# Performance work log

Hardware: AMD Instinct MI355X
Metric: run time of the kernel (lower is better)

## Reference

```python
import jax, jax.numpy as jnp
import numpy as np


def setup_inputs() -> dict:
    key = jax.random.key(0)
    k0, k1, k2, k3, k4 = jax.random.split(key, 5)
    T, B, I, H = 1024, 128, 256, 256
    x = jax.random.normal(k0, (T, B, I), dtype=jnp.float32)
    h0 = jax.random.normal(k1, (1, B, H), dtype=jnp.float32)
    # prepacked transposed weights, gate order [r|z|n] along the 3H axis
    wihT = jax.random.normal(k2, (I, 3 * H), dtype=jnp.float32) * 0.05
    whhT = jax.random.normal(k3, (H, 3 * H), dtype=jnp.float32) * 0.05
    b = jax.random.normal(k4, (3 * H,), dtype=jnp.float32) * 0.05  # fused b_ih + b_hh
    return {"x": x, "h0": h0, "wihT": wihT, "whhT": whhT, "b": b}


def reference(x, h0, wihT, whhT, b):
    # Single-layer GRU recurrence, matching the fused CUDA kernel math:
    #   r = sigmoid(x Wir + h Whr + b_r)
    #   z = sigmoid(x Wiz + h Whz + b_z)
    #   h' = (1 - z) * n + z * h
    H = h0.shape[-1]
    br, bz, bn = b[:H], b[H:2 * H], b[2 * H:]

    def step(h, xt):
        gi = xt @ wihT   # (B, 3H)
        gh = h @ whhT    # (B, 3H)
        r = jax.nn.sigmoid(gi[:, :H] + gh[:, :H] + br)
        z = jax.nn.sigmoid(gi[:, H:2 * H] + gh[:, H:2 * H] + bz)
        n = jnp.tanh(gi[:, 2 * H:] + bn + r * gh[:, 2 * H:])
        h_new = (1.0 - z) * n + z * h
        return h_new, None

    h_final, _ = jax.lax.scan(step, h0[0], x)  # scan over T
    return h_final[None]  # (1, B, H)
```

## Files before the change

### kernel.cpp

```cpp
#include <hip/hip_runtime.h>
#include <hip/hip_fp16.h>

#define TT 1024
#define BB 128
#define II 256
#define HH 256
#define NG 768

__device__ __align__(16) unsigned short g_xbf[(size_t)TT * BB * II];
__device__ __align__(16) unsigned short g_wihB[NG * II];
__device__ __align__(16) _Float16       g_gi[(size_t)TT * BB * NG];

typedef __attribute__((ext_vector_type(8))) short    bfrag;
typedef __attribute__((ext_vector_type(8))) _Float16 hfrag;
typedef __attribute__((ext_vector_type(4))) float    f32x4;

__device__ __forceinline__ unsigned short f2bf(float f) {
    unsigned u = __float_as_uint(f);
    return (unsigned short)((u + 0x7fffu + ((u >> 16) & 1u)) >> 16);
}

__global__ void cvt_x_kernel(const float* __restrict__ x) {
    const int n4 = TT * BB * II / 4;
    for (int i = blockIdx.x * blockDim.x + threadIdx.x; i < n4;
         i += gridDim.x * blockDim.x) {
        float4 v = reinterpret_cast<const float4*>(x)[i];
        ushort4 o;
        o.x = f2bf(v.x); o.y = f2bf(v.y); o.z = f2bf(v.z); o.w = f2bf(v.w);
        reinterpret_cast<ushort4*>(g_xbf)[i] = o;
    }
}

__global__ void cvt_wih_kernel(const float* __restrict__ wihT) {
    const int n = blockIdx.x;
    const int k = threadIdx.x;
    g_wihB[n * II + k] = f2bf(wihT[k * NG + n]);
}

__global__ void __launch_bounds__(256) gi_gemm_kernel(const float* __restrict__ bias) {
    __shared__ unsigned short Ab[128 * 32];
    __shared__ unsigned short Bb[128 * 32];
    const int tid = threadIdx.x;
    const int mt = blockIdx.x / 6, nt = blockIdx.x % 6;
    const int m0 = mt * 128, n0 = nt * 128;
    const int l = tid & 63, w = tid >> 6;
    const int wr = w >> 1, wc = w & 1;
    const int srow = tid >> 2, scol = (tid & 3) * 8;

    f32x4 acc[4][4] = {};

    for (int ks = 0; ks < 8; ++ks) {
        const int k0 = ks * 32;
        __syncthreads();
        #pragma unroll
        for (int c = 0; c < 2; ++c) {
            const int row = c * 64 + srow;
            *reinterpret_cast<uint4*>(&Ab[row * 32 + scol]) =
                *reinterpret_cast<const uint4*>(&g_xbf[(size_t)(m0 + row) * II + k0 + scol]);
            *reinterpret_cast<uint4*>(&Bb[row * 32 + scol]) =
                *reinterpret_cast<const uint4*>(&g_wihB[(n0 + row) * II + k0 + scol]);
        }
        __syncthreads();
        bfrag af[4], bf[4];
        #pragma unroll
        for (int i = 0; i < 4; ++i) {
            af[i] = *reinterpret_cast<const bfrag*>(
                        &Ab[(wr * 64 + i * 16 + (l & 15)) * 32 + (l >> 4) * 8]);
            bf[i] = *reinterpret_cast<const bfrag*>(
                        &Bb[(wc * 64 + i * 16 + (l & 15)) * 32 + (l >> 4) * 8]);
        }
        #pragma unroll
        for (int mi = 0; mi < 4; ++mi)
            #pragma unroll
            for (int ni = 0; ni < 4; ++ni)
                acc[mi][ni] = __builtin_amdgcn_mfma_f32_16x16x32_bf16(
                                  af[mi], bf[ni], acc[mi][ni], 0, 0, 0);
    }
    #pragma unroll
    for (int mi = 0; mi < 4; ++mi) {
        const int grow = m0 + wr * 64 + mi * 16 + (l >> 4) * 4;
        #pragma unroll
        for (int ni = 0; ni < 4; ++ni) {
            const int gcol = n0 + wc * 64 + ni * 16 + (l & 15);
            const float bv = bias[gcol];
            #pragma unroll
            for (int q = 0; q < 4; ++q)
                g_gi[(size_t)(grow + q) * NG + gcol] = (_Float16)(acc[mi][ni][q] + bv);
        }
    }
}

#define LDB(NAME, CB, KT)                                                   \
    hfrag NAME;                                                             \
    _Pragma("unroll")                                                       \
    for (int e = 0; e < 8; ++e)                                             \
        NAME[e] = (_Float16)whhT[(size_t)((KT) * 32 + g * 8 + e) * NG + (CB) + ln15];

#define KSTEP(KT)                                                           \
    {                                                                       \
        const hfrag Av = *reinterpret_cast<const hfrag*>(hl + (KT) * 32 + (g << 3)); \
        const hfrag A  = (ln15 == 0) ? Av : hz;                             \
        accR = __builtin_amdgcn_mfma_f32_16x16x32_f16(A, BR##KT, accR, 0, 0, 0); \
        accZ = __builtin_amdgcn_mfma_f32_16x16x32_f16(A, BZ##KT, accZ, 0, 0, 0); \
        accN = __builtin_amdgcn_mfma_f32_16x16x32_f16(A, BN##KT, accN, 0, 0, 0); \
    }

__global__ void __launch_bounds__(1024)
__attribute__((amdgpu_waves_per_eu(4, 4)))
gru_rec_kernel(
    const float* __restrict__ h0, const float* __restrict__ whhT,
    float* __restrict__ out)
{
    __shared__ __align__(16) _Float16 hbuf[2][HH];

    const int tid  = threadIdx.x;
    const int b    = blockIdx.x;
    const int w    = tid >> 6;
    const int l    = tid & 63;
    const int g    = l >> 4;
    const int ln15 = l & 15;
    const int jb   = w << 4;
    const int jj   = jb + ln15;

    LDB(BR0, jb, 0) LDB(BR1, jb, 1) LDB(BR2, jb, 2) LDB(BR3, jb, 3)
    LDB(BR4, jb, 4) LDB(BR5, jb, 5) LDB(BR6, jb, 6) LDB(BR7, jb, 7)
    LDB(BZ0, HH + jb, 0) LDB(BZ1, HH + jb, 1) LDB(BZ2, HH + jb, 2) LDB(BZ3, HH + jb, 3)
    LDB(BZ4, HH + jb, 4) LDB(BZ5, HH + jb, 5) LDB(BZ6, HH + jb, 6) LDB(BZ7, HH + jb, 7)
    LDB(BN0, 2*HH + jb, 0) LDB(BN1, 2*HH + jb, 1) LDB(BN2, 2*HH + jb, 2) LDB(BN3, 2*HH + jb, 3)
    LDB(BN4, 2*HH + jb, 4) LDB(BN5, 2*HH + jb, 5) LDB(BN6, 2*HH + jb, 6) LDB(BN7, 2*HH + jb, 7)

    const hfrag hz = {};

    float hprev = h0[b * HH + jj];
    if (tid < 256) hbuf[0][tid] = (_Float16)h0[b * HH + tid];
    __syncthreads();

    const _Float16* gb0 = g_gi + (size_t)b * NG;
    float gR = (float)gb0[jj], gZ = (float)gb0[HH + jj], gN = (float)gb0[2 * HH + jj];

    for (int t = 0; t < TT; ++t) {
        const _Float16* hl  = hbuf[t & 1];
        _Float16*       hn_ = hbuf[(t & 1) ^ 1];

        float nR = gR, nZ = gZ, nN = gN;
        if (t + 1 < TT) {
            const _Float16* gn = g_gi + ((size_t)(t + 1) * BB + b) * NG;
            nR = (float)gn[jj]; nZ = (float)gn[HH + jj]; nN = (float)gn[2 * HH + jj];
        }

        f32x4 accR = {0.f, 0.f, 0.f, 0.f};
        f32x4 accZ = {0.f, 0.f, 0.f, 0.f};
        f32x4 accN = {0.f, 0.f, 0.f, 0.f};
        KSTEP(0) KSTEP(1) KSTEP(2) KSTEP(3)
        KSTEP(4) KSTEP(5) KSTEP(6) KSTEP(7)

        const float r  = 1.f / (1.f + __expf(-(accR[0] + gR)));
        const float z  = 1.f / (1.f + __expf(-(accZ[0] + gZ)));
        const float e  = __expf(2.f * (gN + r * accN[0]));
        const float n  = 1.f - 2.f / (e + 1.f);
        const float hv = (1.f - z) * n + z * hprev;
        if (g == 0) {
            hprev = hv;
            hn_[jj] = (_Float16)hv;
            if (t == TT - 1) out[b * HH + jj] = hv;
        }

        gR = nR; gZ = nZ; gN = nN;
        __syncthreads();
    }
}

extern "C" void kernel_launch(void* const* d_in, const int* in_sizes, int n_in,
                              void* d_out, int out_size, void* d_ws, size_t ws_size,
                              hipStream_t stream) {
    const float* x    = (const float*)d_in[0];
    const float* h0   = (const float*)d_in[1];
    const float* wihT = (const float*)d_in[2];
    const float* whhT = (const float*)d_in[3];
    const float* bias = (const float*)d_in[4];
    float*       out  = (float*)d_out;

    cvt_x_kernel<<<2048, 256, 0, stream>>>(x);
    cvt_wih_kernel<<<NG, 256, 0, stream>>>(wihT);
    gi_gemm_kernel<<<1024 * 6, 256, 0, stream>>>(bias);
    gru_rec_kernel<<<BB, 1024, 0, stream>>>(h0, whhT, out);
}
```

Before: 1.502 ms.

## Halve recurrence block to 512 threads, each wave owning two hidden column tiles

The GRU recurrence kernel now runs 8 waves per block instead of 16. Each wave computes two 16-column tiles for each of the three gates, so it issues six MFMA chains per k-step instead of three. The 48 weight fragments per lane are pinned in AccVGPRs with an inline-asm constraint so they fit in the register file at 2 waves per EU. The aim is cheaper per-step __syncthreads across fewer waves and more independent MFMA work per wave. The cost is a longer serial chain per wave and register pressure.

```diff
diff --git a/kernel.cpp b/kernel.cpp
--- a/kernel.cpp
+++ b/kernel.cpp
@@ -90,23 +90,30 @@
     }
 }
 
-#define LDB(NAME, CB, KT)                                                   \
-    hfrag NAME;                                                             \
+#define LDB1(T, KT)                                                         \
+    hfrag B##T##_##KT;                                                      \
     _Pragma("unroll")                                                       \
     for (int e = 0; e < 8; ++e)                                             \
-        NAME[e] = (_Float16)whhT[(size_t)((KT) * 32 + g * 8 + e) * NG + (CB) + ln15];
-
-#define KSTEP(KT)                                                           \
+        B##T##_##KT[e] = (_Float16)whhT[(size_t)((KT) * 32 + g8 + e) * NG + cb##T + ln15]; \
+    asm("" : "+a"(B##T##_##KT));
+
+#define LDB8(T) LDB1(T,0) LDB1(T,1) LDB1(T,2) LDB1(T,3) \
+                LDB1(T,4) LDB1(T,5) LDB1(T,6) LDB1(T,7)
+
+#define KST(KT)                                                             \
     {                                                                       \
-        const hfrag Av = *reinterpret_cast<const hfrag*>(hl + (KT) * 32 + (g << 3)); \
+        const hfrag Av = *reinterpret_cast<const hfrag*>(hl + (KT) * 32 + g8); \
         const hfrag A  = (ln15 == 0) ? Av : hz;                             \
-        accR = __builtin_amdgcn_mfma_f32_16x16x32_f16(A, BR##KT, accR, 0, 0, 0); \
-        accZ = __builtin_amdgcn_mfma_f32_16x16x32_f16(A, BZ##KT, accZ, 0, 0, 0); \
-        accN = __builtin_amdgcn_mfma_f32_16x16x32_f16(A, BN##KT, accN, 0, 0, 0); \
-    }
-
-__global__ void __launch_bounds__(1024)
-__attribute__((amdgpu_waves_per_eu(4, 4)))
+        acc0 = __builtin_amdgcn_mfma_f32_16x16x32_f16(A, B0_##KT, acc0, 0, 0, 0); \
+        acc1 = __builtin_amdgcn_mfma_f32_16x16x32_f16(A, B1_##KT, acc1, 0, 0, 0); \
+        acc2 = __builtin_amdgcn_mfma_f32_16x16x32_f16(A, B2_##KT, acc2, 0, 0, 0); \
+        acc3 = __builtin_amdgcn_mfma_f32_16x16x32_f16(A, B3_##KT, acc3, 0, 0, 0); \
+        acc4 = __builtin_amdgcn_mfma_f32_16x16x32_f16(A, B4_##KT, acc4, 0, 0, 0); \
+        acc5 = __builtin_amdgcn_mfma_f32_16x16x32_f16(A, B5_##KT, acc5, 0, 0, 0); \
+    }
+
+__global__ void __launch_bounds__(512)
+__attribute__((amdgpu_waves_per_eu(2, 2)))
 gru_rec_kernel(
     const float* __restrict__ h0, const float* __restrict__ whhT,
     float* __restrict__ out)
@@ -117,55 +124,70 @@
     const int b    = blockIdx.x;
     const int w    = tid >> 6;
     const int l    = tid & 63;
-    const int g    = l >> 4;
     const int ln15 = l & 15;
-    const int jb   = w << 4;
-    const int jj   = jb + ln15;
-
-    LDB(BR0, jb, 0) LDB(BR1, jb, 1) LDB(BR2, jb, 2) LDB(BR3, jb, 3)
-    LDB(BR4, jb, 4) LDB(BR5, jb, 5) LDB(BR6, jb, 6) LDB(BR7, jb, 7)
-    LDB(BZ0, HH + jb, 0) LDB(BZ1, HH + jb, 1) LDB(BZ2, HH + jb, 2) LDB(BZ3, HH + jb, 3)
-    LDB(BZ4, HH + jb, 4) LDB(BZ5, HH + jb, 5) LDB(BZ6, HH + jb, 6) LDB(BZ7, HH + jb, 7)
-    LDB(BN0, 2*HH + jb, 0) LDB(BN1, 2*HH + jb, 1) LDB(BN2, 2*HH + jb, 2) LDB(BN3, 2*HH + jb, 3)
-    LDB(BN4, 2*HH + jb, 4) LDB(BN5, 2*HH + jb, 5) LDB(BN6, 2*HH + jb, 6) LDB(BN7, 2*HH + jb, 7)
+    const int g8   = (l >> 4) * 8;
+    const int cb0 = (w)      * 16;
+    const int cb1 = (w + 8)  * 16;
+    const int cb2 = (w + 16) * 16;
+    const int cb3 = (w + 24) * 16;
+    const int cb4 = (w + 32) * 16;
+    const int cb5 = (w + 40) * 16;
+    const int jj1 = w * 16 + ln15;
+    const int jj2 = jj1 + 128;
+
+    LDB8(0) LDB8(1) LDB8(2) LDB8(3) LDB8(4) LDB8(5)
 
     const hfrag hz = {};
 
-    float hprev = h0[b * HH + jj];
+    float hprev1 = h0[b * HH + jj1];
+    float hprev2 = h0[b * HH + jj2];
     if (tid < 256) hbuf[0][tid] = (_Float16)h0[b * HH + tid];
     __syncthreads();
 
     const _Float16* gb0 = g_gi + (size_t)b * NG;
-    float gR = (float)gb0[jj], gZ = (float)gb0[HH + jj], gN = (float)gb0[2 * HH + jj];
+    float gR1 = (float)gb0[jj1], gZ1 = (float)gb0[HH + jj1], gN1 = (float)gb0[2 * HH + jj1];
+    float gR2 = (float)gb0[jj2], gZ2 = (float)gb0[HH + jj2], gN2 = (float)gb0[2 * HH + jj2];
 
     for (int t = 0; t < TT; ++t) {
         const _Float16* hl  = hbuf[t & 1];
         _Float16*       hn_ = hbuf[(t & 1) ^ 1];
 
-        float nR = gR, nZ = gZ, nN = gN;
+        float nR1 = gR1, nZ1 = gZ1, nN1 = gN1, nR2 = gR2, nZ2 = gZ2, nN2 = gN2;
         if (t + 1 < TT) {
             const _Float16* gn = g_gi + ((size_t)(t + 1) * BB + b) * NG;
-            nR = (float)gn[jj]; nZ = (float)gn[HH + jj]; nN = (float)gn[2 * HH + jj];
-        }
-
-        f32x4 accR = {0.f, 0.f, 0.f, 0.f};
-        f32x4 accZ = {0.f, 0.f, 0.f, 0.f};
-        f32x4 accN = {0.f, 0.f, 0.f, 0.f};
-        KSTEP(0) KSTEP(1) KSTEP(2) KSTEP(3)
-        KSTEP(4) KSTEP(5) KSTEP(6) KSTEP(7)
-
-        const float r  = 1.f / (1.f + __expf(-(accR[0] + gR)));
-        const float z  = 1.f / (1.f + __expf(-(accZ[0] + gZ)));
-        const float e  = __expf(2.f * (gN + r * accN[0]));
-        const float n  = 1.f - 2.f / (e + 1.f);
-        const float hv = (1.f - z) * n + z * hprev;
-        if (g == 0) {
-            hprev = hv;
-            hn_[jj] = (_Float16)hv;
-            if (t == TT - 1) out[b * HH + jj] = hv;
-        }
-
-        gR = nR; gZ = nZ; gN = nN;
+            nR1 = (float)gn[jj1]; nZ1 = (float)gn[HH + jj1]; nN1 = (float)gn[2 * HH + jj1];
+            nR2 = (float)gn[jj2]; nZ2 = (float)gn[HH + jj2]; nN2 = (float)gn[2 * HH + jj2];
+        }
+
+        f32x4 acc0 = {0.f,0.f,0.f,0.f}, acc1 = {0.f,0.f,0.f,0.f};
+        f32x4 acc2 = {0.f,0.f,0.f,0.f}, acc3 = {0.f,0.f,0.f,0.f};
+        f32x4 acc4 = {0.f,0.f,0.f,0.f}, acc5 = {0.f,0.f,0.f,0.f};
+        KST(0) KST(1) KST(2) KST(3) KST(4) KST(5) KST(6) KST(7)
+
+        const float r1 = 1.f / (1.f + __expf(-(acc0[0] + gR1)));
+        const float z1 = 1.f / (1.f + __expf(-(acc2[0] + gZ1)));
+        const float e1 = __expf(2.f * (gN1 + r1 * acc4[0]));
+        const float n1 = 1.f - 2.f / (e1 + 1.f);
+        const float hv1 = (1.f - z1) * n1 + z1 * hprev1;
+
+        const float r2 = 1.f / (1.f + __expf(-(acc1[0] + gR2)));
+        const float z2 = 1.f / (1.f + __expf(-(acc3[0] + gZ2)));
+        const float e2 = __expf(2.f * (gN2 + r2 * acc5[0]));
+        const float n2 = 1.f - 2.f / (e2 + 1.f);
+        const float hv2 = (1.f - z2) * n2 + z2 * hprev2;
+
+        if ((l >> 4) == 0) {
+            hprev1 = hv1; hprev2 = hv2;
+            hn_[jj1] = (_Float16)hv1;
+            hn_[jj2] = (_Float16)hv2;
+            if (t == TT - 1) {
+                out[b * HH + jj1] = hv1;
+                out[b * HH + jj2] = hv2;
+            }
+        }
+
+        gR1 = nR1; gZ1 = nZ1; gN1 = nN1;
+        gR2 = nR2; gZ2 = nZ2; gN2 = nN2;
         __syncthreads();
     }
 }
@@ -183,5 +205,5 @@
     cvt_x_kernel<<<2048, 256, 0, stream>>>(x);
     cvt_wih_kernel<<<NG, 256, 0, stream>>>(wihT);
     gi_gemm_kernel<<<1024 * 6, 256, 0, stream>>>(bias);
-    gru_rec_kernel<<<BB, 1024, 0, stream>>>(h0, whhT, out);
-}
+    gru_rec_kernel<<<BB, 512, 0, stream>>>(h0, whhT, out);
+}
```

New measurement: 3.459 ms. 2.3x slower.

## Replace MFMA matvec in GRU recurrence with fdot2 over register/LDS-split weights

Applied to the files above, without the earlier changes.

The recurrent kernel used 16x16x32 MFMAs in which only one row of A was non-zero, so most of the matrix-unit work was wasted. It now computes h·Whh with packed fp16 fdot2 instructions, with each of 512 threads handling one output column and one half of K. The packed weights are split three ways: 96 dwords per thread in registers, 78 in LDS, and 18 re-read from global memory every step. A new pack kernel prepares this layout, and a shared partial-sum exchange with two barriers per step combines the K halves. The risks are high register pressure, LDS bandwidth on every step, and global reloads of the spilled weights.

```diff
diff --git a/kernel.cpp b/kernel.cpp
--- a/kernel.cpp
+++ b/kernel.cpp
@@ -10,14 +10,19 @@
 __device__ __align__(16) unsigned short g_xbf[(size_t)TT * BB * II];
 __device__ __align__(16) unsigned short g_wihB[NG * II];
 __device__ __align__(16) _Float16       g_gi[(size_t)TT * BB * NG];
-
-typedef __attribute__((ext_vector_type(8))) short    bfrag;
-typedef __attribute__((ext_vector_type(8))) _Float16 hfrag;
-typedef __attribute__((ext_vector_type(4))) float    f32x4;
+__device__ __align__(16) unsigned       g_wpk[192 * 512];
+
+typedef __attribute__((ext_vector_type(8)))  short    bfrag;
+typedef __attribute__((ext_vector_type(4)))  float    f32x4;
+typedef __attribute__((ext_vector_type(2)))  _Float16 h2t;
+typedef __attribute__((ext_vector_type(32))) unsigned u32x32;
 
 __device__ __forceinline__ unsigned short f2bf(float f) {
     unsigned u = __float_as_uint(f);
     return (unsigned short)((u + 0x7fffu + ((u >> 16) & 1u)) >> 16);
+}
+__device__ __forceinline__ unsigned pk2(float a, float b) {
+    return __builtin_bit_cast(unsigned, __builtin_amdgcn_cvt_pkrtz(a, b));
 }
 
 __global__ void cvt_x_kernel(const float* __restrict__ x) {
@@ -35,6 +40,28 @@
     const int n = blockIdx.x;
     const int k = threadIdx.x;
     g_wihB[n * II + k] = f2bf(wihT[k * NG + n]);
+}
+
+__global__ void pack_whh_kernel(const float* __restrict__ whhT) {
+    const int wt = blockIdx.x;
+    const int t  = threadIdx.x;
+    const int kh = t >> 8, j = t & 255;
+    const int pl = wt / 3, gate = wt % 3;
+    const int p  = kh * 64 + pl;
+    const int c  = gate * HH + j;
+    const unsigned val = pk2(whhT[(size_t)(2 * p) * NG + c],
+                             whhT[(size_t)(2 * p + 1) * NG + c]);
+    size_t addr;
+    if (wt < 96) {
+        addr = (size_t)wt * 512 + t;
+    } else if (wt < 174) {
+        const int lw = wt - 96;
+        if (lw < 76) addr = 96 * 512 + (size_t)(lw >> 2) * 2048 + t * 4 + (lw & 3);
+        else         addr = 96 * 512 + 76 * 512 + t * 2 + (lw - 76);
+    } else {
+        addr = 174 * 512 + (size_t)t * 18 + (wt - 174);
+    }
+    g_wpk[addr] = val;
 }
 
 __global__ void __launch_bounds__(256) gi_gemm_kernel(const float* __restrict__ bias) {
@@ -90,82 +117,113 @@
     }
 }
 
-#define LDB(NAME, CB, KT)                                                   \
-    hfrag NAME;                                                             \
-    _Pragma("unroll")                                                       \
-    for (int e = 0; e < 8; ++e)                                             \
-        NAME[e] = (_Float16)whhT[(size_t)((KT) * 32 + g * 8 + e) * NG + (CB) + ln15];
-
-#define KSTEP(KT)                                                           \
-    {                                                                       \
-        const hfrag Av = *reinterpret_cast<const hfrag*>(hl + (KT) * 32 + (g << 3)); \
-        const hfrag A  = (ln15 == 0) ? Av : hz;                             \
-        accR = __builtin_amdgcn_mfma_f32_16x16x32_f16(A, BR##KT, accR, 0, 0, 0); \
-        accZ = __builtin_amdgcn_mfma_f32_16x16x32_f16(A, BZ##KT, accZ, 0, 0, 0); \
-        accN = __builtin_amdgcn_mfma_f32_16x16x32_f16(A, BN##KT, accN, 0, 0, 0); \
-    }
-
-__global__ void __launch_bounds__(1024)
-__attribute__((amdgpu_waves_per_eu(4, 4)))
-gru_rec_kernel(
-    const float* __restrict__ h0, const float* __restrict__ whhT,
-    float* __restrict__ out)
+#define FD(HH2, W, ACC) \
+    ACC = __builtin_amdgcn_fdot2((HH2), __builtin_bit_cast(h2t, (unsigned)(W)), (ACC), false)
+
+#define WGET(W) ((W) < 32 ? wv0[(W) & 31] : (W) < 64 ? wv1[(W) & 31] : wv2[(W) & 31])
+
+#define HREAD(PL)                                                             \
+    { const uint2 hb = *reinterpret_cast<const uint2*>(                       \
+          reinterpret_cast<const _Float16*>(hbuf) + kh * 128 + (PL) * 2);     \
+      hx = hb.x; hy = hb.y; }
+
+#define DOT3(HW, W0, W1, W2)                                                  \
+    { const h2t hh = __builtin_bit_cast(h2t, (unsigned)(HW));                 \
+      FD(hh, W0, aR); FD(hh, W1, aZ); FD(hh, W2, aN); }
+
+#define DREG(PL, HW) DOT3(HW, WGET(3*(PL)), WGET(3*(PL)+1), WGET(3*(PL)+2))
+#define R2(PL) HREAD(PL) DREG(PL, hx) DREG((PL)+1, hy)
+
+#define LQ(Q) (*reinterpret_cast<const uint4*>(&ldsw[(Q) * 2048 + t * 4]))
+
+#define LBLK(PB)                                                              \
+    { const uint4 q0 = LQ(3*(PB)); const uint4 q1 = LQ(3*(PB)+1);             \
+      const uint4 q2 = LQ(3*(PB)+2);                                          \
+      HREAD(32 + 4*(PB))                                                      \
+      DOT3(hx, q0.x, q0.y, q0.z)  DOT3(hy, q0.w, q1.x, q1.y)                  \
+      HREAD(34 + 4*(PB))                                                      \
+      DOT3(hx, q1.z, q1.w, q2.x)  DOT3(hy, q2.y, q2.z, q2.w) }
+
+__global__ void __launch_bounds__(512) gru_rec_kernel(
+    const float* __restrict__ h0, float* __restrict__ out)
 {
-    __shared__ __align__(16) _Float16 hbuf[2][HH];
-
-    const int tid  = threadIdx.x;
-    const int b    = blockIdx.x;
-    const int w    = tid >> 6;
-    const int l    = tid & 63;
-    const int g    = l >> 4;
-    const int ln15 = l & 15;
-    const int jb   = w << 4;
-    const int jj   = jb + ln15;
-
-    LDB(BR0, jb, 0) LDB(BR1, jb, 1) LDB(BR2, jb, 2) LDB(BR3, jb, 3)
-    LDB(BR4, jb, 4) LDB(BR5, jb, 5) LDB(BR6, jb, 6) LDB(BR7, jb, 7)
-    LDB(BZ0, HH + jb, 0) LDB(BZ1, HH + jb, 1) LDB(BZ2, HH + jb, 2) LDB(BZ3, HH + jb, 3)
-    LDB(BZ4, HH + jb, 4) LDB(BZ5, HH + jb, 5) LDB(BZ6, HH + jb, 6) LDB(BZ7, HH + jb, 7)
-    LDB(BN0, 2*HH + jb, 0) LDB(BN1, 2*HH + jb, 1) LDB(BN2, 2*HH + jb, 2) LDB(BN3, 2*HH + jb, 3)
-    LDB(BN4, 2*HH + jb, 4) LDB(BN5, 2*HH + jb, 5) LDB(BN6, 2*HH + jb, 6) LDB(BN7, 2*HH + jb, 7)
-
-    const hfrag hz = {};
-
-    float hprev = h0[b * HH + jj];
-    if (tid < 256) hbuf[0][tid] = (_Float16)h0[b * HH + tid];
+    __shared__ __align__(16) unsigned ldsw[78 * 512];
+    __shared__ float    part[3][256];
+    __shared__ _Float16 hbuf[256];
+
+    const int t  = threadIdx.x;
+    const int b  = blockIdx.x;
+    const int kh = t >> 8;
+    const int j  = t & 255;
+
+    u32x32 wv0, wv1, wv2;
+    #pragma unroll
+    for (int e = 0; e < 32; ++e) {
+        wv0[e] = g_wpk[(size_t)(e)      * 512 + t];
+        wv1[e] = g_wpk[(size_t)(32 + e) * 512 + t];
+        wv2[e] = g_wpk[(size_t)(64 + e) * 512 + t];
+    }
+
+    {
+        uint4* lq = reinterpret_cast<uint4*>(ldsw);
+        const uint4* gq = reinterpret_cast<const uint4*>(g_wpk + 96 * 512);
+        for (int i = t; i < 78 * 512 / 4; i += 512) lq[i] = gq[i];
+    }
+
+    float hprev = h0[b * HH + j];
+    if (t < 256) hbuf[t] = (_Float16)h0[b * HH + t];
     __syncthreads();
 
-    const _Float16* gb0 = g_gi + (size_t)b * NG;
-    float gR = (float)gb0[jj], gZ = (float)gb0[HH + jj], gN = (float)gb0[2 * HH + jj];
-
-    for (int t = 0; t < TT; ++t) {
-        const _Float16* hl  = hbuf[t & 1];
-        _Float16*       hn_ = hbuf[(t & 1) ^ 1];
-
-        float nR = gR, nZ = gZ, nN = gN;
-        if (t + 1 < TT) {
-            const _Float16* gn = g_gi + ((size_t)(t + 1) * BB + b) * NG;
-            nR = (float)gn[jj]; nZ = (float)gn[HH + jj]; nN = (float)gn[2 * HH + jj];
-        }
-
-        f32x4 accR = {0.f, 0.f, 0.f, 0.f};
-        f32x4 accZ = {0.f, 0.f, 0.f, 0.f};
-        f32x4 accN = {0.f, 0.f, 0.f, 0.f};
-        KSTEP(0) KSTEP(1) KSTEP(2) KSTEP(3)
-        KSTEP(4) KSTEP(5) KSTEP(6) KSTEP(7)
-
-        const float r  = 1.f / (1.f + __expf(-(accR[0] + gR)));
-        const float z  = 1.f / (1.f + __expf(-(accZ[0] + gZ)));
-        const float e  = __expf(2.f * (gN + r * accN[0]));
-        const float n  = 1.f - 2.f / (e + 1.f);
-        const float hv = (1.f - z) * n + z * hprev;
-        if (g == 0) {
+    const unsigned* sbase = g_wpk + 174 * 512 + (size_t)t * 18;
+
+    for (int ts = 0; ts < TT; ++ts) {
+        unsigned s0 = sbase[0],  s1 = sbase[1],  s2 = sbase[2],  s3 = sbase[3];
+        unsigned s4 = sbase[4],  s5 = sbase[5],  s6 = sbase[6],  s7 = sbase[7];
+        unsigned s8 = sbase[8],  s9 = sbase[9],  s10 = sbase[10], s11 = sbase[11];
+        unsigned s12 = sbase[12], s13 = sbase[13], s14 = sbase[14], s15 = sbase[15];
+        unsigned s16 = sbase[16], s17 = sbase[17];
+        float giR = 0.f, giZ = 0.f, giN = 0.f;
+        if (kh == 0) {
+            const _Float16* gb = g_gi + ((size_t)ts * BB + b) * NG + j;
+            giR = (float)gb[0]; giZ = (float)gb[256]; giN = (float)gb[512];
+        }
+
+        float aR = 0.f, aZ = 0.f, aN = 0.f;
+        unsigned hx, hy;
+
+        R2(0)  R2(2)  R2(4)  R2(6)  R2(8)  R2(10) R2(12) R2(14)
+        R2(16) R2(18) R2(20) R2(22) R2(24) R2(26) R2(28) R2(30)
+
+        HREAD(58) DOT3(hx, s0, s1, s2)    DOT3(hy, s3, s4, s5)
+        HREAD(60) DOT3(hx, s6, s7, s8)    DOT3(hy, s9, s10, s11)
+        HREAD(62) DOT3(hx, s12, s13, s14) DOT3(hy, s15, s16, s17)
+
+        LBLK(0) LBLK(1) LBLK(2) LBLK(3) LBLK(4) LBLK(5)
+        {
+            const uint4 q = LQ(18);
+            const uint2 b2 = *reinterpret_cast<const uint2*>(&ldsw[76 * 512 + t * 2]);
+            HREAD(56)
+            DOT3(hx, q.x, q.y, q.z)
+            DOT3(hy, q.w, b2.x, b2.y)
+        }
+
+        if (kh == 1) {
+            part[0][j] = aR; part[1][j] = aZ; part[2][j] = aN;
+        }
+        __syncthreads();
+        if (kh == 0) {
+            const float sR = aR + part[0][j];
+            const float sZ = aZ + part[1][j];
+            const float sN = aN + part[2][j];
+            const float r = 1.f / (1.f + __expf(-(sR + giR)));
+            const float z = 1.f / (1.f + __expf(-(sZ + giZ)));
+            const float e = __expf(2.f * (giN + r * sN));
+            const float n = 1.f - 2.f / (e + 1.f);
+            const float hv = (1.f - z) * n + z * hprev;
             hprev = hv;
-            hn_[jj] = (_Float16)hv;
-            if (t == TT - 1) out[b * HH + jj] = hv;
-        }
-
-        gR = nR; gZ = nZ; gN = nN;
+            hbuf[j] = (_Float16)hv;
+            if (ts == TT - 1) out[b * HH + j] = hv;
+        }
         __syncthreads();
     }
 }
@@ -182,6 +240,7 @@
 
     cvt_x_kernel<<<2048, 256, 0, stream>>>(x);
     cvt_wih_kernel<<<NG, 256, 0, stream>>>(wihT);
+    pack_whh_kernel<<<192, 512, 0, stream>>>(whhT);
     gi_gemm_kernel<<<1024 * 6, 256, 0, stream>>>(bias);
-    gru_rec_kernel<<<BB, 1024, 0, stream>>>(h0, whhT, out);
-}
+    gru_rec_kernel<<<BB, 512, 0, stream>>>(h0, out);
+}
```

Result: slower. 1.646 ms (+9.6%).

## Shrink GRU recurrence block to 4 waves, each owning four hidden tiles

Applied to the files above, without the earlier changes.

The recurrent kernel now runs with 256 threads per batch row instead of 1024. Each wave holds weights for four 16-column tiles per gate and issues twelve MFMAs per k-step, with half the weight fragments pinned into AGPRs through inline asm. Fewer waves should make each per-timestep barrier cheaper and reduce scheduling overhead. In exchange, each wave carries four times the serial MFMA chain and far more register pressure, with a risk of spilling.

```diff
diff --git a/kernel.cpp b/kernel.cpp
--- a/kernel.cpp
+++ b/kernel.cpp
@@ -90,82 +90,139 @@
     }
 }
 
-#define LDB(NAME, CB, KT)                                                   \
+#define MF(A, B, C) __builtin_amdgcn_mfma_f32_16x16x32_f16((A), (B), (C), 0, 0, 0)
+
+#define LDB1(NAME, GATE, TB, KT)                                            \
     hfrag NAME;                                                             \
     _Pragma("unroll")                                                       \
     for (int e = 0; e < 8; ++e)                                             \
-        NAME[e] = (_Float16)whhT[(size_t)((KT) * 32 + g * 8 + e) * NG + (CB) + ln15];
-
-#define KSTEP(KT)                                                           \
+        NAME[e] = (_Float16)whhT[(size_t)((KT) * 32 + g8 + e) * NG          \
+                                 + (GATE) * HH + (TB) + ln15];
+
+#define DECL8(P, GATE, I, TB)                                               \
+    LDB1(P##I##_0, GATE, TB, 0) LDB1(P##I##_1, GATE, TB, 1)                 \
+    LDB1(P##I##_2, GATE, TB, 2) LDB1(P##I##_3, GATE, TB, 3)                 \
+    LDB1(P##I##_4, GATE, TB, 4) LDB1(P##I##_5, GATE, TB, 5)                 \
+    LDB1(P##I##_6, GATE, TB, 6) LDB1(P##I##_7, GATE, TB, 7)
+
+#define PIN8(P, I)                                                          \
+    asm("" : "+a"(P##I##_0)); asm("" : "+a"(P##I##_1));                     \
+    asm("" : "+a"(P##I##_2)); asm("" : "+a"(P##I##_3));                     \
+    asm("" : "+a"(P##I##_4)); asm("" : "+a"(P##I##_5));                     \
+    asm("" : "+a"(P##I##_6)); asm("" : "+a"(P##I##_7));
+
+#define KST(KT)                                                             \
     {                                                                       \
-        const hfrag Av = *reinterpret_cast<const hfrag*>(hl + (KT) * 32 + (g << 3)); \
+        const hfrag Av = *reinterpret_cast<const hfrag*>(hl + (KT) * 32 + g8); \
         const hfrag A  = (ln15 == 0) ? Av : hz;                             \
-        accR = __builtin_amdgcn_mfma_f32_16x16x32_f16(A, BR##KT, accR, 0, 0, 0); \
-        accZ = __builtin_amdgcn_mfma_f32_16x16x32_f16(A, BZ##KT, accZ, 0, 0, 0); \
-        accN = __builtin_amdgcn_mfma_f32_16x16x32_f16(A, BN##KT, accN, 0, 0, 0); \
-    }
-
-__global__ void __launch_bounds__(1024)
-__attribute__((amdgpu_waves_per_eu(4, 4)))
-gru_rec_kernel(
+        aR0 = MF(A, BR0_##KT, aR0); aR1 = MF(A, BR1_##KT, aR1);             \
+        aR2 = MF(A, BR2_##KT, aR2); aR3 = MF(A, BR3_##KT, aR3);             \
+        aZ0 = MF(A, BZ0_##KT, aZ0); aZ1 = MF(A, BZ1_##KT, aZ1);             \
+        aZ2 = MF(A, BZ2_##KT, aZ2); aZ3 = MF(A, BZ3_##KT, aZ3);             \
+        aN0 = MF(A, BN0_##KT, aN0); aN1 = MF(A, BN1_##KT, aN1);             \
+        aN2 = MF(A, BN2_##KT, aN2); aN3 = MF(A, BN3_##KT, aN3);             \
+    }
+
+__global__ void __launch_bounds__(256, 1) gru_rec_kernel(
     const float* __restrict__ h0, const float* __restrict__ whhT,
     float* __restrict__ out)
 {
     __shared__ __align__(16) _Float16 hbuf[2][HH];
 
-    const int tid  = threadIdx.x;
+    const int t    = threadIdx.x;
     const int b    = blockIdx.x;
-    const int w    = tid >> 6;
-    const int l    = tid & 63;
-    const int g    = l >> 4;
+    const int w    = t >> 6;
+    const int l    = t & 63;
     const int ln15 = l & 15;
-    const int jb   = w << 4;
-    const int jj   = jb + ln15;
-
-    LDB(BR0, jb, 0) LDB(BR1, jb, 1) LDB(BR2, jb, 2) LDB(BR3, jb, 3)
-    LDB(BR4, jb, 4) LDB(BR5, jb, 5) LDB(BR6, jb, 6) LDB(BR7, jb, 7)
-    LDB(BZ0, HH + jb, 0) LDB(BZ1, HH + jb, 1) LDB(BZ2, HH + jb, 2) LDB(BZ3, HH + jb, 3)
-    LDB(BZ4, HH + jb, 4) LDB(BZ5, HH + jb, 5) LDB(BZ6, HH + jb, 6) LDB(BZ7, HH + jb, 7)
-    LDB(BN0, 2*HH + jb, 0) LDB(BN1, 2*HH + jb, 1) LDB(BN2, 2*HH + jb, 2) LDB(BN3, 2*HH + jb, 3)
-    LDB(BN4, 2*HH + jb, 4) LDB(BN5, 2*HH + jb, 5) LDB(BN6, 2*HH + jb, 6) LDB(BN7, 2*HH + jb, 7)
+    const int g8   = (l >> 4) * 8;
+    const int tb0  = (4 * w + 0) * 16, tb1 = (4 * w + 1) * 16;
+    const int tb2  = (4 * w + 2) * 16, tb3 = (4 * w + 3) * 16;
+    const int j0 = tb0 + ln15, j1 = tb1 + ln15, j2 = tb2 + ln15, j3 = tb3 + ln15;
+
+    DECL8(BR, 0, 0, tb0) PIN8(BR, 0)  DECL8(BR, 0, 1, tb1) PIN8(BR, 1)
+    DECL8(BR, 0, 2, tb2) PIN8(BR, 2)  DECL8(BR, 0, 3, tb3) PIN8(BR, 3)
+    DECL8(BZ, 1, 0, tb0) PIN8(BZ, 0)  DECL8(BZ, 1, 1, tb1) PIN8(BZ, 1)
+    DECL8(BZ, 1, 2, tb2) PIN8(BZ, 2)  DECL8(BZ, 1, 3, tb3) PIN8(BZ, 3)
+    DECL8(BN, 2, 0, tb0)              DECL8(BN, 2, 1, tb1)
+    DECL8(BN, 2, 2, tb2)              DECL8(BN, 2, 3, tb3)
 
     const hfrag hz = {};
-
-    float hprev = h0[b * HH + jj];
-    if (tid < 256) hbuf[0][tid] = (_Float16)h0[b * HH + tid];
+    const int gq = l >> 4;
+
+    float hp0 = h0[b * HH + j0], hp1 = h0[b * HH + j1];
+    float hp2 = h0[b * HH + j2], hp3 = h0[b * HH + j3];
+    hbuf[0][t] = (_Float16)h0[b * HH + t];
     __syncthreads();
 
-    const _Float16* gb0 = g_gi + (size_t)b * NG;
-    float gR = (float)gb0[jj], gZ = (float)gb0[HH + jj], gN = (float)gb0[2 * HH + jj];
-
-    for (int t = 0; t < TT; ++t) {
-        const _Float16* hl  = hbuf[t & 1];
-        _Float16*       hn_ = hbuf[(t & 1) ^ 1];
-
-        float nR = gR, nZ = gZ, nN = gN;
-        if (t + 1 < TT) {
-            const _Float16* gn = g_gi + ((size_t)(t + 1) * BB + b) * NG;
-            nR = (float)gn[jj]; nZ = (float)gn[HH + jj]; nN = (float)gn[2 * HH + jj];
-        }
-
-        f32x4 accR = {0.f, 0.f, 0.f, 0.f};
-        f32x4 accZ = {0.f, 0.f, 0.f, 0.f};
-        f32x4 accN = {0.f, 0.f, 0.f, 0.f};
-        KSTEP(0) KSTEP(1) KSTEP(2) KSTEP(3)
-        KSTEP(4) KSTEP(5) KSTEP(6) KSTEP(7)
-
-        const float r  = 1.f / (1.f + __expf(-(accR[0] + gR)));
-        const float z  = 1.f / (1.f + __expf(-(accZ[0] + gZ)));
-        const float e  = __expf(2.f * (gN + r * accN[0]));
-        const float n  = 1.f - 2.f / (e + 1.f);
-        const float hv = (1.f - z) * n + z * hprev;
-        if (g == 0) {
-            hprev = hv;
-            hn_[jj] = (_Float16)hv;
-            if (t == TT - 1) out[b * HH + jj] = hv;
-        }
-
-        gR = nR; gZ = nZ; gN = nN;
+    float gR0 = 0.f, gR1 = 0.f, gR2 = 0.f, gR3 = 0.f;
+    float gZ0 = 0.f, gZ1 = 0.f, gZ2 = 0.f, gZ3 = 0.f;
+    float gN0 = 0.f, gN1 = 0.f, gN2 = 0.f, gN3 = 0.f;
+    if (gq == 0) {
+        const _Float16* gb = g_gi + (size_t)b * NG;
+        gR0 = (float)gb[j0]; gR1 = (float)gb[j1]; gR2 = (float)gb[j2]; gR3 = (float)gb[j3];
+        gZ0 = (float)gb[256 + j0]; gZ1 = (float)gb[256 + j1];
+        gZ2 = (float)gb[256 + j2]; gZ3 = (float)gb[256 + j3];
+        gN0 = (float)gb[512 + j0]; gN1 = (float)gb[512 + j1];
+        gN2 = (float)gb[512 + j2]; gN3 = (float)gb[512 + j3];
+    }
+
+    for (int ts = 0; ts < TT; ++ts) {
+        const _Float16* hl  = hbuf[ts & 1];
+        _Float16*       hn_ = hbuf[(ts & 1) ^ 1];
+
+        float nR0 = gR0, nR1 = gR1, nR2 = gR2, nR3 = gR3;
+        float nZ0 = gZ0, nZ1 = gZ1, nZ2 = gZ2, nZ3 = gZ3;
+        float nN0 = gN0, nN1 = gN1, nN2 = gN2, nN3 = gN3;
+        if (gq == 0 && ts + 1 < TT) {
+            const _Float16* gn = g_gi + ((size_t)(ts + 1) * BB + b) * NG;
+            nR0 = (float)gn[j0]; nR1 = (float)gn[j1]; nR2 = (float)gn[j2]; nR3 = (float)gn[j3];
+            nZ0 = (float)gn[256 + j0]; nZ1 = (float)gn[256 + j1];
+            nZ2 = (float)gn[256 + j2]; nZ3 = (float)gn[256 + j3];
+            nN0 = (float)gn[512 + j0]; nN1 = (float)gn[512 + j1];
+            nN2 = (float)gn[512 + j2]; nN3 = (float)gn[512 + j3];
+        }
+
+        f32x4 aR0 = {0.f,0.f,0.f,0.f}, aR1 = {0.f,0.f,0.f,0.f};
+        f32x4 aR2 = {0.f,0.f,0.f,0.f}, aR3 = {0.f,0.f,0.f,0.f};
+        f32x4 aZ0 = {0.f,0.f,0.f,0.f}, aZ1 = {0.f,0.f,0.f,0.f};
+        f32x4 aZ2 = {0.f,0.f,0.f,0.f}, aZ3 = {0.f,0.f,0.f,0.f};
+        f32x4 aN0 = {0.f,0.f,0.f,0.f}, aN1 = {0.f,0.f,0.f,0.f};
+        f32x4 aN2 = {0.f,0.f,0.f,0.f}, aN3 = {0.f,0.f,0.f,0.f};
+        KST(0) KST(1) KST(2) KST(3) KST(4) KST(5) KST(6) KST(7)
+
+        const float r0 = 1.f / (1.f + __expf(-(aR0[0] + gR0)));
+        const float z0 = 1.f / (1.f + __expf(-(aZ0[0] + gZ0)));
+        const float e0 = __expf(2.f * (gN0 + r0 * aN0[0]));
+        const float hv0 = (1.f - z0) * (1.f - 2.f / (e0 + 1.f)) + z0 * hp0;
+
+        const float r1 = 1.f / (1.f + __expf(-(aR1[0] + gR1)));
+        const float z1 = 1.f / (1.f + __expf(-(aZ1[0] + gZ1)));
+        const float e1 = __expf(2.f * (gN1 + r1 * aN1[0]));
+        const float hv1 = (1.f - z1) * (1.f - 2.f / (e1 + 1.f)) + z1 * hp1;
+
+        const float r2 = 1.f / (1.f + __expf(-(aR2[0] + gR2)));
+        const float z2 = 1.f / (1.f + __expf(-(aZ2[0] + gZ2)));
+        const float e2 = __expf(2.f * (gN2 + r2 * aN2[0]));
+        const float hv2 = (1.f - z2) * (1.f - 2.f / (e2 + 1.f)) + z2 * hp2;
+
+        const float r3 = 1.f / (1.f + __expf(-(aR3[0] + gR3)));
+        const float z3 = 1.f / (1.f + __expf(-(aZ3[0] + gZ3)));
+        const float e3 = __expf(2.f * (gN3 + r3 * aN3[0]));
+        const float hv3 = (1.f - z3) * (1.f - 2.f / (e3 + 1.f)) + z3 * hp3;
+
+        if (gq == 0) {
+            hp0 = hv0; hp1 = hv1; hp2 = hv2; hp3 = hv3;
+            hn_[j0] = (_Float16)hv0; hn_[j1] = (_Float16)hv1;
+            hn_[j2] = (_Float16)hv2; hn_[j3] = (_Float16)hv3;
+            if (ts == TT - 1) {
+                out[b * HH + j0] = hv0; out[b * HH + j1] = hv1;
+                out[b * HH + j2] = hv2; out[b * HH + j3] = hv3;
+            }
+        }
+
+        gR0 = nR0; gR1 = nR1; gR2 = nR2; gR3 = nR3;
+        gZ0 = nZ0; gZ1 = nZ1; gZ2 = nZ2; gZ3 = nZ3;
+        gN0 = nN0; gN1 = nN1; gN2 = nN2; gN3 = nN3;
         __syncthreads();
     }
 }
@@ -183,5 +240,5 @@
     cvt_x_kernel<<<2048, 256, 0, stream>>>(x);
     cvt_wih_kernel<<<NG, 256, 0, stream>>>(wihT);
     gi_gemm_kernel<<<1024 * 6, 256, 0, stream>>>(bias);
-    gru_rec_kernel<<<BB, 1024, 0, stream>>>(h0, whhT, out);
-}
+    gru_rec_kernel<<<BB, 256, 0, stream>>>(h0, whhT, out);
+}
```

Result: slower. 2.338 ms (+55.7%).
